# Performance work log

Measured on AMD Instinct MI355X. Metric: run time of the kernel, lower is better.

The kernel has to match this reference:

```python
import jax, jax.numpy as jnp
import numpy as np

N = 2048        # n_nodes
FIN = 512       # in_features
FOUT = 256      # out_features
ALPHA = 0.25
EPS = 1e-4
TOPK = 32
MAX_ITERS = 200
AVG_DEG = 16.0


def _glorot(key, shape, gain=1.414):
    fan_in, fan_out = shape[0], shape[-1]
    s = gain * (6.0 / (fan_in + fan_out)) ** 0.5
    return jax.random.uniform(key, shape, jnp.float32, -s, s)


def setup_inputs() -> dict:
    key = jax.random.key(0)
    k1, k2, k3, k4, k5 = jax.random.split(key, 5)
    h = jax.random.normal(k1, (N, FIN), jnp.float32)
    # random Bernoulli graph with avg degree ~AVG_DEG, plus self-loops so deg >= 1
    adj = (jax.random.uniform(k2, (N, N)) < (AVG_DEG / N)).astype(jnp.float32)
    adj = jnp.maximum(adj, jnp.eye(N, dtype=jnp.float32))
    W = _glorot(k3, (FIN, FOUT))
    a = _glorot(k4, (2 * FOUT, 1))
    a_ppr = _glorot(k5, (1, 1))
    return {"h": h, "adj": adj, "W": W, "a": a, "a_ppr": a_ppr}


def compute_ppr_topk(adj):
    """Parallel (synchronous) forward-push PPR for all source nodes at once,
    followed by per-row top-k sparsification and symmetric degree rescaling.
    Same math/fixed-point as the sequential queue-based push in the original."""
    deg = adj.sum(1)                       # [N]
    thr = ALPHA * EPS * deg                # push threshold per target node

    def cond(c):
        _, R, it = c
        return jnp.logical_and(jnp.any(R >= thr[None, :]), it < MAX_ITERS)

    def body(c):
        P, R, it = c
        push = jnp.where(R >= thr[None, :], R, 0.0)   # [N_src, N]
        P = P + push
        # spread (1-alpha)*res/deg[u] along edges u->v for all sources in parallel
        R = R - push + (1.0 - ALPHA) * ((push / deg[None, :]) @ adj)
        return (P, R, it + 1)

    P0 = jnp.zeros((N, N), jnp.float32)
    R0 = ALPHA * jnp.eye(N, dtype=jnp.float32)        # r[src, src] = alpha
    P, _, _ = jax.lax.while_loop(cond, body, (P0, R0, 0))

    vals, idx = jax.lax.top_k(P, TOPK)                # [N, TOPK]
    rows = jnp.arange(N)[:, None]
    ppr = jnp.zeros((N, N), jnp.float32).at[rows, idx].set(vals)
    deg_s = jnp.sqrt(jnp.clip(deg, 1e-12))
    # multiply nonzeros by deg_sqrt[row] * deg_inv_sqrt[col]; zeros stay zero
    ppr = ppr * (deg_s[:, None] / deg_s[None, :])
    return ppr


def reference(h, adj, W, a, a_ppr):
    ppr = compute_ppr_topk(adj)
    HW = h @ W                                        # [N, FOUT]
    h1 = HW @ a[:FOUT, :]                             # [N, 1]
    h2 = HW @ a[FOUT:, :]                             # [N, 1]
    e = h1 + h2.T + a_ppr * ppr                       # [N, N]
    e = jax.nn.leaky_relu(e, 0.2)
    att = jnp.where(adj > 0, e, jnp.float32(-9e15))
    att = jax.nn.softmax(att, axis=1)
    return att @ HW                                   # [N, FOUT]
```

## Files before the change

### kernel.cpp

```cpp
#include <hip/hip_runtime.h>


typedef unsigned short u16;
typedef unsigned int u32;
typedef float  f32x4  __attribute__((ext_vector_type(4)));
typedef short  s16x8  __attribute__((ext_vector_type(8)));
typedef __bf16 bf16x8 __attribute__((ext_vector_type(8)));

#define NN 2048

__device__ __forceinline__ u16 f2bf(float f) {
    unsigned u = __float_as_uint(f);
    return (u16)((u + 0x7FFFu + ((u >> 16) & 1u)) >> 16);
}
__device__ __forceinline__ float bf2f(u16 v) {
    return __uint_as_float(((unsigned)v) << 16);
}

__global__ __launch_bounds__(256, 5)
void build_kernel(const float* __restrict__ adj, const float* __restrict__ h,
                  const float* __restrict__ W, const float* __restrict__ av,
                  unsigned char* __restrict__ BMb, float* __restrict__ cbf,
                  float* __restrict__ deg,
                  float* __restrict__ HW, float* __restrict__ h1part,
                  float* __restrict__ h2part) {
    __shared__ __align__(16) u16 As[2][64 * 64];
    __shared__ __align__(16) u16 Bs[2][64 * 64];
    __shared__ float red[8];
    const int tid = threadIdx.x, lane = tid & 63, wid = tid >> 6;

    if (blockIdx.x >= 128) {
        const int row = blockIdx.x - 128;
        const float* ar = adj + (size_t)row * NN;
        const int j0 = tid * 8;
        f32x4 a0 = *(const f32x4*)(ar + j0), a1 = *(const f32x4*)(ar + j0 + 4);
        float s = a0[0] + a0[1] + a0[2] + a0[3] + a1[0] + a1[1] + a1[2] + a1[3];
        #pragma unroll
        for (int o = 32; o; o >>= 1) s += __shfl_down(s, o);
        if (lane == 0) red[wid] = s;
        __syncthreads();
        const float t = red[0] + red[1] + red[2] + red[3];
        if (tid == 0) {
            deg[row] = t;
            cbf[row] = bf2f(f2bf(0.75f * (1.0f / t)));
        }
        unsigned bb = 0;
        #pragma unroll
        for (int j = 0; j < 4; j++) bb |= (a0[j] > 0.f) ? (1u << j) : 0u;
        #pragma unroll
        for (int j = 0; j < 4; j++) bb |= (a1[j] > 0.f) ? (1u << (4 + j)) : 0u;
        BMb[(size_t)row * 256 + (tid & 63) * 4 + (tid >> 6)] = (unsigned char)bb;
        return;
    }

    const int b2 = blockIdx.x;
    const int trow = (b2 >> 2) * 64, tcol = (b2 & 3) * 64;
    const int wrow = (wid >> 1) * 32, wcol = (wid & 1) * 32;
    const int lrow = lane & 15, lq = lane >> 4;

    const int arow = tid >> 2, aq = tid & 3;
    auto stageA = [&](int k0, int buf) {
        const float* hp = h + (size_t)(trow + arow) * 512 + k0 + aq * 16;
        f32x4 v0 = *(const f32x4*)hp;
        f32x4 v1 = *(const f32x4*)(hp + 4);
        f32x4 v2 = *(const f32x4*)(hp + 8);
        f32x4 v3 = *(const f32x4*)(hp + 12);
        union { u16 h[8]; uint4 q; } o0, o1;
        #pragma unroll
        for (int j = 0; j < 4; j++) {
            o0.h[j] = f2bf(v0[j]); o0.h[4 + j] = f2bf(v1[j]);
            o1.h[j] = f2bf(v2[j]); o1.h[4 + j] = f2bf(v3[j]);
        }
        const int g0 = aq * 2;
        *(uint4*)&As[buf][arow * 64 + (g0 ^ (arow & 7)) * 8]       = o0.q;
        *(uint4*)&As[buf][arow * 64 + ((g0 + 1) ^ (arow & 7)) * 8] = o1.q;
    };
    const int bcol = tid >> 2, bq = tid & 3;
    auto stageB = [&](int k0, int buf) {
        union { u16 h[8]; uint4 q; } o0, o1;
        #pragma unroll
        for (int j = 0; j < 8; j++) {
            o0.h[j] = f2bf(W[(size_t)(k0 + bq * 16 + j) * 256 + tcol + bcol]);
            o1.h[j] = f2bf(W[(size_t)(k0 + bq * 16 + 8 + j) * 256 + tcol + bcol]);
        }
        const int g0 = bq * 2;
        *(uint4*)&Bs[buf][bcol * 64 + (g0 ^ (bcol & 7)) * 8]       = o0.q;
        *(uint4*)&Bs[buf][bcol * 64 + ((g0 + 1) ^ (bcol & 7)) * 8] = o1.q;
    };

    f32x4 acc[2][2] = {};
    stageA(0, 0); stageB(0, 0);
    __syncthreads();
    for (int ks = 0; ks < 8; ks++) {
        const int cur = ks & 1;
        if (ks < 7) { stageA((ks + 1) * 64, cur ^ 1); stageB((ks + 1) * 64, cur ^ 1); }
        bf16x8 af[2][2], bfv[2][2];
        #pragma unroll
        for (int kk = 0; kk < 2; kk++) {
            const int gsz = ((kk * 4 + lq) ^ (lrow & 7)) * 8;
            #pragma unroll
            for (int m = 0; m < 2; m++) {
                af[m][kk]  = *(const bf16x8*)&As[cur][(wrow + m * 16 + lrow) * 64 + gsz];
                bfv[m][kk] = *(const bf16x8*)&Bs[cur][(wcol + m * 16 + lrow) * 64 + gsz];
            }
        }
        #pragma unroll
        for (int kk = 0; kk < 2; kk++)
            #pragma unroll
            for (int m = 0; m < 2; m++)
                #pragma unroll
                for (int n = 0; n < 2; n++)
                    acc[m][n] = __builtin_amdgcn_mfma_f32_16x16x32_bf16(
                        af[m][kk], bfv[n][kk], acc[m][n], 0, 0, 0);
        __syncthreads();
    }
    float* hred = (float*)&As[0][0];
    const int crow0 = trow + wrow + lq * 4;
    const int ccol0 = tcol + wcol + lrow;
    float av1[2], av2[2];
    #pragma unroll
    for (int n = 0; n < 2; n++) {
        av1[n] = av[ccol0 + n * 16];
        av2[n] = av[256 + ccol0 + n * 16];
    }
    #pragma unroll
    for (int m = 0; m < 2; m++) {
        #pragma unroll
        for (int r = 0; r < 4; r++) {
            float s1 = 0.f, s2 = 0.f;
            #pragma unroll
            for (int n = 0; n < 2; n++) {
                const float v = acc[m][n][r];
                HW[(size_t)(crow0 + m * 16 + r) * 256 + ccol0 + n * 16] = v;
                s1 += v * av1[n];
                s2 += v * av2[n];
            }
            #pragma unroll
            for (int o = 1; o < 16; o <<= 1) {
                s1 += __shfl_xor(s1, o);
                s2 += __shfl_xor(s2, o);
            }
            if (lrow == 0) {
                const int rl = wrow + lq * 4 + m * 16 + r;
                hred[rl * 4 + (wid & 1) * 2 + 0] = s1;
                hred[rl * 4 + (wid & 1) * 2 + 1] = s2;
            }
        }
    }
    __syncthreads();
    if (tid < 64) {
        h1part[(size_t)(b2 & 3) * NN + trow + tid] = hred[tid * 4 + 0] + hred[tid * 4 + 2];
        h2part[(size_t)(b2 & 3) * NN + trow + tid] = hred[tid * 4 + 1] + hred[tid * 4 + 3];
    }
}

__device__ __forceinline__ int wred_sum_i(int v) {
    #pragma unroll
    for (int o = 32; o; o >>= 1) v += __shfl_down(v, o);
    return __shfl(v, 0);
}
__device__ __forceinline__ float wred_sum_f(float v) {
    #pragma unroll
    for (int o = 32; o; o >>= 1) v += __shfl_down(v, o);
    return __shfl(v, 0);
}
__device__ __forceinline__ float wred_max_f(float v) {
    #pragma unroll
    for (int o = 32; o; o >>= 1) v = fmaxf(v, __shfl_down(v, o));
    return __shfl(v, 0);
}

__global__ __launch_bounds__(64)
void mega_kernel(const u32* __restrict__ BM, const float* __restrict__ cbf,
                 const float* __restrict__ HW,
                 const float* __restrict__ h1p, const float* __restrict__ h2p,
                 const float* __restrict__ degv,
                 const float* __restrict__ a_ppr_p, float* __restrict__ out) {
    __shared__ int   nidx_[128];
    __shared__ float nmv_[128];
    __shared__ float pval_[128];
    __shared__ float nval_[128];
    const int lane = threadIdx.x;
    const int row = blockIdx.x;
    const float wi = cbf[row];

    const u32 wbits = BM[(size_t)row * 64 + lane];
    int L = 0;
    #pragma unroll
    for (int i = 0; i < 4; i++) {
        const unsigned b = (wbits >> (8 * i)) & 0xffu;
        const int cnt = __popc(b);
        int sc = cnt;
        #pragma unroll
        for (int o = 1; o < 64; o <<= 1) {
            const int t = __shfl_up(sc, o);
            if (lane >= o) sc += t;
        }
        int pos = L + sc - cnt;
        const int j0 = i * 512 + lane * 8;
        #pragma unroll
        for (int e = 0; e < 8; e++)
            if ((b & (1u << e)) && pos < 128) {
                nidx_[pos] = j0 + e; nmv_[pos] = cbf[j0 + e]; pos++;
            }
        L += __shfl(sc, 63);
    }
    if (L > 128) L = 128;
    __syncthreads();

    const bool vA = (lane < L), vB = (lane + 64 < L);
    const int jA = vA ? nidx_[lane] : 0;
    const int jB = vB ? nidx_[lane + 64] : 0;
    const int wAi = (jA >> 3) & 63, bAi = ((jA >> 9) << 3) | (jA & 7);
    const int wBi = (jB >> 3) & 63, bBi = ((jB >> 9) << 3) | (jB & 7);
    float pA = wi; if (vA && jA == row) pA += 1.f;
    float pB = wi; if (vB && jB == row) pB += 1.f;

    u32 w0 = BM[(size_t)nidx_[0] * 64 + lane];
    u32 w1 = (L > 1) ? BM[(size_t)nidx_[1] * 64 + lane] : 0u;
    u32 w2 = (L > 2) ? BM[(size_t)nidx_[2] * 64 + lane] : 0u;
    for (int kk = 0; kk < L; kk++) {
        const u32 wb = w0;
        w0 = w1; w1 = w2;
        w2 = (kk + 3 < L) ? BM[(size_t)nidx_[kk + 3] * 64 + lane] : 0u;
        const float ck = nmv_[kk];
        const u32 wordA = __shfl(wb, wAi);
        const u32 wordB = __shfl(wb, wBi);
        pA = fmaf(wi, ((wordA >> bAi) & 1u) ? ck : 0.f, pA);
        pB = fmaf(wi, ((wordB >> bBi) & 1u) ? ck : 0.f, pB);
    }
    pA *= 0.25f; pB *= 0.25f;
    if (vA) pval_[lane] = pA;
    if (vB) pval_[lane + 64] = pB;

    float cut = -1.0f;
    int tsel = 32, te = 0;
    if (L > 32) {
        unsigned lo = 0u, hi = 0x40000000u;
        while (hi - lo > 1u) {
            const unsigned mid = (lo + hi) >> 1;
            const float mf = __uint_as_float(mid);
            int c = (vA && pA >= mf) + (vB && pB >= mf);
            c = wred_sum_i(c);
            if (c >= 32) lo = mid; else hi = mid;
        }
        cut = __uint_as_float(lo);
        int mg = (vA && pA > cut) + (vB && pB > cut);
        int t2 = (vA && pA == cut) + (vB && pB == cut);
        mg = wred_sum_i(mg);
        te = wred_sum_i(t2);
        tsel = 32 - mg;
    }

    __syncthreads();

    const float dgr = degv[row];
    const float apr = a_ppr_p[0];
    const float h1r = h1p[row] + h1p[NN + row] + h1p[2 * NN + row] + h1p[3 * NN + row];
    float mymax = -3.0e38f;
    for (int k = lane; k < L; k += 64) {
        const int j = nidx_[k];
        const float p = pval_[k];
        bool sel = p > cut;
        if (!sel && p == cut) {
            if (tsel >= te) sel = true;
            else {
                int rk = 0;
                for (int q = 0; q < k; q++) rk += (pval_[q] == cut);
                sel = (rk < tsel);
            }
        }
        const float h2j = h2p[j] + h2p[NN + j] + h2p[2 * NN + j] + h2p[3 * NN + j];
        const float pprv = sel ? p * sqrtf(dgr / degv[j]) : 0.f;
        float e = h1r + h2j + apr * pprv;
        e = (e > 0.f) ? e : 0.2f * e;
        nval_[k] = e;
        mymax = fmaxf(mymax, e);
    }
    const float mx = wred_max_f(mymax);
    float mysum = 0.f;
    for (int k = lane; k < L; k += 64) {
        const float ev = expf(nval_[k] - mx);
        nval_[k] = ev;
        mysum += ev;
    }
    const float inv = 1.f / wred_sum_f(mysum);

    __syncthreads();

    f32x4 acc = {0.f, 0.f, 0.f, 0.f};
    for (int k = 0; k < L; k++) {
        const float a = nval_[k] * inv;
        const int j = nidx_[k];
        f32x4 hv = *(const f32x4*)(HW + (size_t)j * 256 + lane * 4);
        acc += a * hv;
    }
    *(f32x4*)(out + (size_t)row * 256 + lane * 4) = acc;
}

extern "C" void kernel_launch(void* const* d_in, const int* in_sizes, int n_in,
                              void* d_out, int out_size, void* d_ws, size_t ws_size,
                              hipStream_t stream) {
    const float* h     = (const float*)d_in[0];
    const float* adj   = (const float*)d_in[1];
    const float* W     = (const float*)d_in[2];
    const float* a     = (const float*)d_in[3];
    const float* a_ppr = (const float*)d_in[4];
    float* out = (float*)d_out;

    char* ws = (char*)d_ws;
    auto alloc = [&](size_t bytes) { char* p = ws; ws += (bytes + 255) & ~(size_t)255; return p; };
    unsigned char* BMb = (unsigned char*)alloc((size_t)NN * 256);
    float* cbf    = (float*)alloc(NN * 4);
    float* HW     = (float*)alloc((size_t)NN * 256 * 4);
    float* deg    = (float*)alloc(NN * 4);
    float* h1part = (float*)alloc((size_t)4 * NN * 4);
    float* h2part = (float*)alloc((size_t)4 * NN * 4);

    build_kernel<<<2176, 256, 0, stream>>>(adj, h, W, a, BMb, cbf, deg,
                                           HW, h1part, h2part);
    mega_kernel<<<NN, 64, 0, stream>>>((const u32*)BMb, cbf, HW,
                                       h1part, h2part, deg, a_ppr, out);
}
```

Measured before the change: 37.20 us.

## Precompute CSR neighbor lists in build kernel and stage neighbor bitmaps in LDS

The adjacency row pass in the build kernel now also emits a compact per-row neighbor index list (up to 128) and its count, so the main kernel no longer rebuilds it with four wave scans over the bitmap. The main kernel bulk-loads up to 64 neighbor bitmap rows into a 16KB shared array and reads bits from LDS instead of using cross-lane shuffles on a register pipeline. It also adds a 4-deep register prefetch of HW rows in the final aggregation loop. The cost is extra global writes and reads for the CSR arrays, plus more LDS per 64-thread block, which may limit how many blocks fit per CU.

```diff
diff --git a/kernel.cpp b/kernel.cpp
--- a/kernel.cpp
+++ b/kernel.cpp
@@ -20,7 +20,8 @@
 __global__ __launch_bounds__(256, 5)
 void build_kernel(const float* __restrict__ adj, const float* __restrict__ h,
                   const float* __restrict__ W, const float* __restrict__ av,
-                  unsigned char* __restrict__ BMb, float* __restrict__ cbf,
+                  unsigned char* __restrict__ BMb, u16* __restrict__ CSRc,
+                  int* __restrict__ NL, float* __restrict__ cbf,
                   float* __restrict__ deg,
                   float* __restrict__ HW, float* __restrict__ h1part,
                   float* __restrict__ h2part) {
@@ -49,7 +50,29 @@
         for (int j = 0; j < 4; j++) bb |= (a0[j] > 0.f) ? (1u << j) : 0u;
         #pragma unroll
         for (int j = 0; j < 4; j++) bb |= (a1[j] > 0.f) ? (1u << (4 + j)) : 0u;
-        BMb[(size_t)row * 256 + (tid & 63) * 4 + (tid >> 6)] = (unsigned char)bb;
+        BMb[(size_t)row * 256 + lane * 4 + wid] = (unsigned char)bb;
+
+        int* wsumi = (int*)&Bs[0][0];
+        const int cnt = __popc(bb);
+        int sc = cnt;
+        #pragma unroll
+        for (int o = 1; o < 64; o <<= 1) {
+            const int tt = __shfl_up(sc, o);
+            if (lane >= o) sc += tt;
+        }
+        if (lane == 63) wsumi[wid] = sc;
+        __syncthreads();
+        int base = 0;
+        #pragma unroll
+        for (int w = 0; w < 4; w++) if (w < wid) base += wsumi[w];
+        int pos = base + sc - cnt;
+        #pragma unroll
+        for (int e = 0; e < 8; e++)
+            if ((bb & (1u << e)) && pos < 128) CSRc[(size_t)row * 128 + pos++] = (u16)(j0 + e);
+        if (tid == 0) {
+            int Lt = wsumi[0] + wsumi[1] + wsumi[2] + wsumi[3];
+            NL[row] = (Lt > 128) ? 128 : Lt;
+        }
         return;
     }
 
@@ -172,10 +195,12 @@
 
 __global__ __launch_bounds__(64)
 void mega_kernel(const u32* __restrict__ BM, const float* __restrict__ cbf,
+                 const u16* __restrict__ CSRc, const int* __restrict__ NL,
                  const float* __restrict__ HW,
                  const float* __restrict__ h1p, const float* __restrict__ h2p,
                  const float* __restrict__ degv,
                  const float* __restrict__ a_ppr_p, float* __restrict__ out) {
+    __shared__ u32   WBM[64][64];
     __shared__ int   nidx_[128];
     __shared__ float nmv_[128];
     __shared__ float pval_[128];
@@ -183,51 +208,37 @@
     const int lane = threadIdx.x;
     const int row = blockIdx.x;
     const float wi = cbf[row];
-
-    const u32 wbits = BM[(size_t)row * 64 + lane];
-    int L = 0;
-    #pragma unroll
-    for (int i = 0; i < 4; i++) {
-        const unsigned b = (wbits >> (8 * i)) & 0xffu;
-        const int cnt = __popc(b);
-        int sc = cnt;
-        #pragma unroll
-        for (int o = 1; o < 64; o <<= 1) {
-            const int t = __shfl_up(sc, o);
-            if (lane >= o) sc += t;
-        }
-        int pos = L + sc - cnt;
-        const int j0 = i * 512 + lane * 8;
-        #pragma unroll
-        for (int e = 0; e < 8; e++)
-            if ((b & (1u << e)) && pos < 128) {
-                nidx_[pos] = j0 + e; nmv_[pos] = cbf[j0 + e]; pos++;
-            }
-        L += __shfl(sc, 63);
-    }
-    if (L > 128) L = 128;
-    __syncthreads();
+    const int L = NL[row];
 
     const bool vA = (lane < L), vB = (lane + 64 < L);
-    const int jA = vA ? nidx_[lane] : 0;
-    const int jB = vB ? nidx_[lane + 64] : 0;
+    int jA = 0, jB = 0;
+    if (vA) jA = CSRc[(size_t)row * 128 + lane];
+    if (vB) jB = CSRc[(size_t)row * 128 + 64 + lane];
+    if (vA) { nidx_[lane] = jA; nmv_[lane] = cbf[jA]; }
+    if (vB) { nidx_[lane + 64] = jB; nmv_[lane + 64] = cbf[jB]; }
+    __syncthreads();
+
+    const int Lp = (L < 64) ? L : 64;
+    for (int kk = 0; kk < Lp; kk++)
+        WBM[kk][lane] = BM[(size_t)nidx_[kk] * 64 + lane];
+    __syncthreads();
+
     const int wAi = (jA >> 3) & 63, bAi = ((jA >> 9) << 3) | (jA & 7);
     const int wBi = (jB >> 3) & 63, bBi = ((jB >> 9) << 3) | (jB & 7);
     float pA = wi; if (vA && jA == row) pA += 1.f;
     float pB = wi; if (vB && jB == row) pB += 1.f;
-
-    u32 w0 = BM[(size_t)nidx_[0] * 64 + lane];
-    u32 w1 = (L > 1) ? BM[(size_t)nidx_[1] * 64 + lane] : 0u;
-    u32 w2 = (L > 2) ? BM[(size_t)nidx_[2] * 64 + lane] : 0u;
-    for (int kk = 0; kk < L; kk++) {
-        const u32 wb = w0;
-        w0 = w1; w1 = w2;
-        w2 = (kk + 3 < L) ? BM[(size_t)nidx_[kk + 3] * 64 + lane] : 0u;
+    for (int kk = 0; kk < Lp; kk++) {
         const float ck = nmv_[kk];
-        const u32 wordA = __shfl(wb, wAi);
-        const u32 wordB = __shfl(wb, wBi);
+        const u32 wordA = WBM[kk][wAi];
+        const u32 wordB = WBM[kk][wBi];
         pA = fmaf(wi, ((wordA >> bAi) & 1u) ? ck : 0.f, pA);
         pB = fmaf(wi, ((wordB >> bBi) & 1u) ? ck : 0.f, pB);
+    }
+    for (int kk = Lp; kk < L; kk++) {
+        const float ck = nmv_[kk];
+        const u32* rp = BM + (size_t)nidx_[kk] * 64;
+        pA = fmaf(wi, ((rp[wAi] >> bAi) & 1u) ? ck : 0.f, pA);
+        pB = fmaf(wi, ((rp[wBi] >> bBi) & 1u) ? ck : 0.f, pB);
     }
     pA *= 0.25f; pB *= 0.25f;
     if (vA) pval_[lane] = pA;
@@ -289,11 +300,16 @@
     __syncthreads();
 
     f32x4 acc = {0.f, 0.f, 0.f, 0.f};
+    f32x4 hv0 = {0,0,0,0}, hv1 = {0,0,0,0}, hv2 = {0,0,0,0}, hv3 = {0,0,0,0};
+    if (L > 0) hv0 = *(const f32x4*)(HW + (size_t)nidx_[0] * 256 + lane * 4);
+    if (L > 1) hv1 = *(const f32x4*)(HW + (size_t)nidx_[1] * 256 + lane * 4);
+    if (L > 2) hv2 = *(const f32x4*)(HW + (size_t)nidx_[2] * 256 + lane * 4);
+    if (L > 3) hv3 = *(const f32x4*)(HW + (size_t)nidx_[3] * 256 + lane * 4);
     for (int k = 0; k < L; k++) {
-        const float a = nval_[k] * inv;
-        const int j = nidx_[k];
-        f32x4 hv = *(const f32x4*)(HW + (size_t)j * 256 + lane * 4);
-        acc += a * hv;
+        const f32x4 cur = hv0;
+        hv0 = hv1; hv1 = hv2; hv2 = hv3;
+        if (k + 4 < L) hv3 = *(const f32x4*)(HW + (size_t)nidx_[k + 4] * 256 + lane * 4);
+        acc += (nval_[k] * inv) * cur;
     }
     *(f32x4*)(out + (size_t)row * 256 + lane * 4) = acc;
 }
@@ -311,14 +327,16 @@
     char* ws = (char*)d_ws;
     auto alloc = [&](size_t bytes) { char* p = ws; ws += (bytes + 255) & ~(size_t)255; return p; };
     unsigned char* BMb = (unsigned char*)alloc((size_t)NN * 256);
+    u16*   CSRc   = (u16*)  alloc((size_t)NN * 128 * 2);
+    int*   NL     = (int*)  alloc(NN * 4);
     float* cbf    = (float*)alloc(NN * 4);
     float* HW     = (float*)alloc((size_t)NN * 256 * 4);
     float* deg    = (float*)alloc(NN * 4);
     float* h1part = (float*)alloc((size_t)4 * NN * 4);
     float* h2part = (float*)alloc((size_t)4 * NN * 4);
 
-    build_kernel<<<2176, 256, 0, stream>>>(adj, h, W, a, BMb, cbf, deg,
+    build_kernel<<<2176, 256, 0, stream>>>(adj, h, W, a, BMb, CSRc, NL, cbf, deg,
                                            HW, h1part, h2part);
-    mega_kernel<<<NN, 64, 0, stream>>>((const u32*)BMb, cbf, HW,
+    mega_kernel<<<NN, 64, 0, stream>>>((const u32*)BMb, cbf, CSRc, NL, HW,
                                        h1part, h2part, deg, a_ppr, out);
 }
```

New measurement: 31.66 us. 1.17x faster.
